# Kernel tuning notes

Hardware: AMD Instinct MI355X
Metric: run time of the kernel (lower is better)

The kernel has to match this reference:

```python
import jax, jax.numpy as jnp
import numpy as np

BITS = 4
GROUP = 128
IN_F = 4096
OUT_F = 11008
MAXQ = (1 << BITS) - 1  # 15


def setup_inputs() -> dict:
    key = jax.random.key(0)
    k = jax.random.split(key, 5)
    x = jax.random.normal(k[0], (4, 2048, IN_F), dtype=jnp.float32)
    qweight = jax.random.randint(k[1], (IN_F // 32 * BITS, OUT_F), 0, 2**31 - 1, dtype=jnp.int32)
    qzeros = jax.random.randint(k[2], (IN_F // GROUP, OUT_F // 32 * BITS), 0, 2**31 - 1, dtype=jnp.int32)
    scales = jax.random.uniform(k[3], (IN_F // GROUP, OUT_F), dtype=jnp.float32) * 0.01
    bias = jax.random.normal(k[4], (OUT_F,), dtype=jnp.float32)
    return {"x": x, "qweight": qweight, "qzeros": qzeros, "scales": scales, "bias": bias}


def reference(x, qweight, qzeros, scales, bias):
    # wf: bit offsets of the 8 nibbles inside each int32 word
    wf = jnp.arange(0, 32, BITS, dtype=jnp.int32)  # [8]
    # unpack zeros: [G, OUT//8] -> [G, OUT//8, 8] -> [G, OUT]
    zeros = ((qzeros[:, :, None] >> wf[None, None, :]) & MAXQ).reshape(scales.shape)
    # unpack weights: [IN//8, OUT] -> [IN//8, 8, OUT] -> [IN, OUT]
    weight = ((qweight[:, None, :] >> wf[None, :, None]) & MAXQ).reshape(IN_F, OUT_F)
    # group-wise dequant: W = s_g * (q - z_g)
    rep_scales = jnp.repeat(scales, GROUP, axis=0)              # [IN, OUT]
    rep_zeros = jnp.repeat(zeros, GROUP, axis=0).astype(x.dtype)
    W = rep_scales.astype(x.dtype) * (weight.astype(x.dtype) - rep_zeros)
    out = jnp.matmul(x.reshape(-1, IN_F), W)                    # [B*S, OUT]
    out = out.reshape(x.shape[:-1] + (OUT_F,)) + bias
    return out
```

## Files before the change

kernel.cpp:

```cpp
#include <hip/hip_runtime.h>
#include <stdint.h>

#define K_DIM 4096
#define N_DIM 11008
#define M_DIM 8192

constexpr int BM = 128, BN = 128, BK = 64;
constexpr int NT  = K_DIM / BK;
constexpr int NZW = N_DIM / 8;
constexpr int NXT = N_DIM / BN;
constexpr int MXT = M_DIM / BM;
constexpr int NWG = NXT * MXT;
constexpr int TILE_ELEMS = BM * BK;

typedef _Float16 f16x2 __attribute__((ext_vector_type(2)));
typedef _Float16 f16x8 __attribute__((ext_vector_type(8)));
typedef float    f32x4 __attribute__((ext_vector_type(4)));
union H8 { f16x8 v; f16x2 p[4]; };

__device__ __forceinline__ f16x8 dq_word(uint32_t w, f16x2 ss, f16x2 zz) {
    H8 r;
    uint32_t t0 = ( w        & 0x000F000Fu) | 0x64006400u;
    uint32_t t1 = ((w >> 4)  & 0x000F000Fu) | 0x64006400u;
    uint32_t t2 = ((w >> 8)  & 0x000F000Fu) | 0x64006400u;
    uint32_t t3 = ((w >> 12) & 0x000F000Fu) | 0x64006400u;
    r.p[0] = (__builtin_bit_cast(f16x2, t0) - zz) * ss;
    r.p[1] = (__builtin_bit_cast(f16x2, t1) - zz) * ss;
    r.p[2] = (__builtin_bit_cast(f16x2, t2) - zz) * ss;
    r.p[3] = (__builtin_bit_cast(f16x2, t3) - zz) * ss;
    return r.v;
}

__global__ __launch_bounds__(256)
void prep_kernel(const float* __restrict__ x, _Float16* __restrict__ x16) {
    const int b  = blockIdx.x;
    const int mt = b >> 6, kt = b & 63;
    _Float16* dst = x16 + (size_t)b * TILE_ELEMS;
#pragma unroll
    for (int it = 0; it < 4; ++it) {
        const int o   = it * 256 + threadIdx.x;
        const int fk  = o >> 7, row = o & 127;
        const float* src = x + (size_t)(mt * 128 + row) * K_DIM + kt * 64 + fk * 8;
        f32x4 a0 = *(const f32x4*)src;
        f32x4 a1 = *(const f32x4*)(src + 4);
        H8 v;
#pragma unroll
        for (int j = 0; j < 4; ++j)
            v.p[j] = __builtin_bit_cast(f16x2, __builtin_amdgcn_cvt_pkrtz(a0[j], a1[j]));
        *(f16x8*)(dst + (size_t)o * 8) = v.v;
    }
}

#define BARC(N) do {                                                         \
    __builtin_amdgcn_sched_barrier(0);                                       \
    asm volatile("s_waitcnt vmcnt(" #N ") lgkmcnt(0)" ::: "memory");         \
    __builtin_amdgcn_s_barrier();                                            \
    __builtin_amdgcn_sched_barrier(0);                                       \
} while (0)

__global__ __launch_bounds__(256, 4)
void qgemm_dma_kernel(const _Float16* __restrict__ x16, const uint32_t* __restrict__ qw,
                      const uint32_t* __restrict__ qz, const float* __restrict__ sc,
                      const float* __restrict__ bias, float* __restrict__ out)
{
    __shared__ _Float16 As[2 * TILE_ELEMS];

    const int tid  = threadIdx.x;
    const int lid  = (blockIdx.x & 7) * (NWG / 8) + (blockIdx.x >> 3);
    const int mt   = lid / NXT;
    const int n0   = (lid % NXT) * BN;

    const int lane = tid & 63, wid = tid >> 6;
    const int lr = lane & 15, lk = lane >> 4;

    f32x4 acc[8][2];
#pragma unroll
    for (int i = 0; i < 8; ++i)
#pragma unroll
        for (int j = 0; j < 2; ++j) {
            f32x4 z = {0.f, 0.f, 0.f, 0.f};
            acc[i][j] = z;
        }

    uint32_t breg[2][4];
    f16x2    ssv[2], zzv[2];
    float    s_nxt[2];
    uint32_t z_nxt[2];

    const int ncb = n0 + wid * 32 + lr;
    const int shz = 4 * (lr & 7);

    const _Float16* xsrc = x16 + (size_t)mt * (64 * TILE_ELEMS) + tid * 8;
    const uint32_t* qp0 = qw + (size_t)lk * N_DIM + ncb;
    const uint32_t* qp1 = qp0 + (size_t)4 * N_DIM;

#define STAGE(BUF, KT) do {                                                  \
    const _Float16* s_ = xsrc + (size_t)(KT) * TILE_ELEMS;                   \
    _Float16* d_ = &As[(BUF) * TILE_ELEMS + tid * 8];                        \
    _Pragma("unroll") for (int it = 0; it < 4; ++it)                         \
        __builtin_amdgcn_global_load_lds(                                    \
            (const __attribute__((address_space(1))) void*)(s_ + it * 2048), \
            (__attribute__((address_space(3))) void*)(d_ + it * 2048), 16, 0, 0); \
    __builtin_amdgcn_sched_barrier(0);   \
    } while (0)

#define LOADB(SET) do {                                                      \
    breg[SET][0] = qp0[0];  breg[SET][1] = qp0[16];                          \
    breg[SET][2] = qp1[0];  breg[SET][3] = qp1[16];                          \
    qp0 += (size_t)8 * N_DIM; qp1 += (size_t)8 * N_DIM; } while (0)

#define LOADSZ(G) do { _Pragma("unroll") for (int j = 0; j < 2; ++j) {       \
    s_nxt[j] = sc[(size_t)(G) * N_DIM + ncb + j * 16];                       \
    z_nxt[j] = qz[(size_t)(G) * NZW + (ncb >> 3) + j * 2]; } } while (0)

#define MAKESZ() do { _Pragma("unroll") for (int j = 0; j < 2; ++j) {        \
    _Float16 zh = (_Float16)(float)(1024u + ((z_nxt[j] >> shz) & 15u));      \
    _Float16 sh = (_Float16)s_nxt[j];                                        \
    f16x2 sp = {sh, sh}; ssv[j] = sp;                                        \
    f16x2 zp = {zh, zh}; zzv[j] = zp; } } while (0)

#define COMPUTE(BUF, SET) do {                                               \
    _Pragma("unroll") for (int ks = 0; ks < 2; ++ks) {                       \
        f16x8 bf0 = dq_word(breg[SET][ks * 2],     ssv[0], zzv[0]);          \
        f16x8 bf1 = dq_word(breg[SET][ks * 2 + 1], ssv[1], zzv[1]);          \
        const int fo_ = (BUF) * TILE_ELEMS + (ks * 4 + lk) * 1024 + lr * 8;  \
        __builtin_amdgcn_s_setprio(1);                                       \
        _Pragma("unroll") for (int i = 0; i < 8; ++i) {                      \
            f16x8 af_ = *(const f16x8*)&As[fo_ + i * 128];                   \
            acc[i][0] = __builtin_amdgcn_mfma_f32_16x16x32_f16(af_, bf0, acc[i][0], 0, 0, 0); \
            acc[i][1] = __builtin_amdgcn_mfma_f32_16x16x32_f16(af_, bf1, acc[i][1], 0, 0, 0); \
        }                                                                    \
        __builtin_amdgcn_s_setprio(0);                                       \
    } } while (0)

    LOADSZ(0);
    STAGE(0, 0);
    LOADB(0);
    BARC(4);

    for (int kt2 = 0; kt2 < NT / 2; ++kt2) {
        const int t0 = 2 * kt2;
        MAKESZ();
        STAGE(1, t0 + 1);
        LOADB(1);
        COMPUTE(0, 0);
        BARC(4);

        if (kt2 + 1 < NT / 2) {
            STAGE(0, t0 + 2);
            LOADB(0);
            LOADSZ(kt2 + 1);
            COMPUTE(1, 1);
            BARC(8);
        } else {
            COMPUTE(1, 1);
        }
    }

#undef STAGE
#undef LOADB
#undef LOADSZ
#undef MAKESZ
#undef COMPUTE

    const int ccol0 = n0 + wid * 32 + lr;
    float bj[2];
#pragma unroll
    for (int j = 0; j < 2; ++j) bj[j] = bias[ccol0 + j * 16];
    const int m0 = mt * BM;
#pragma unroll
    for (int i = 0; i < 8; ++i) {
        const int rbase = m0 + i * 16 + lk * 4;
#pragma unroll
        for (int j = 0; j < 2; ++j) {
            const int col = ccol0 + j * 16;
#pragma unroll
            for (int r = 0; r < 4; ++r)
                out[(size_t)(rbase + r) * N_DIM + col] = acc[i][j][r] + bj[j];
        }
    }
}

constexpr int FB_LDA = 64;

#define BAR() do {                                           \
    asm volatile("s_waitcnt lgkmcnt(0)" ::: "memory");       \
    __builtin_amdgcn_s_barrier();                            \
    __builtin_amdgcn_sched_barrier(0);                       \
} while (0)

__global__ __launch_bounds__(256, 3)
void qgemm_fb_kernel(const float* __restrict__ x, const uint32_t* __restrict__ qw,
                     const uint32_t* __restrict__ qz, const float* __restrict__ sc,
                     const float* __restrict__ bias, float* __restrict__ out)
{
    __shared__ _Float16 As[2][BM * FB_LDA];

    const int tid  = threadIdx.x;
    const int lid  = (blockIdx.x & 7) * (NWG / 8) + (blockIdx.x >> 3);
    const int m0   = (lid / NXT) * BM;
    const int n0   = (lid % NXT) * BN;

    const int lane = tid & 63, wid = tid >> 6;
    const int lr = lane & 15, lk = lane >> 4;
    const int sw = lr & 7;

    const int arow = tid >> 3;
    const int acp  = tid & 7;
    const int wslot = acp ^ (arow & 7);

    f32x4 acc[8][2];
#pragma unroll
    for (int i = 0; i < 8; ++i)
#pragma unroll
        for (int j = 0; j < 2; ++j) { f32x4 z = {0.f,0.f,0.f,0.f}; acc[i][j] = z; }

    f32x4    aS[4][2];
    uint32_t breg[2][4];
    f16x2    ssv[2], zzv[2];
    float    s_nxt[2];
    uint32_t z_nxt[2];

    const int ncb = n0 + wid * 32 + lr;
    const int shz = 4 * (lr & 7);
    const float* xbase = x + (size_t)(m0 + arow) * K_DIM + acp * 8;

    const uint32_t* qp0 = qw + (size_t)lk * N_DIM + ncb;
    const uint32_t* qp1 = qp0 + (size_t)4 * N_DIM;

#define A_LOAD(KT) do { const float* ap_ = xbase + (KT) * BK;                \
    _Pragma("unroll") for (int i = 0; i < 4; ++i) {                          \
        const float* src_ = ap_ + (size_t)(i * 32) * K_DIM;                  \
        aS[i][0] = *(const f32x4*)(src_);                                    \
        aS[i][1] = *(const f32x4*)(src_ + 4); } } while (0)

#define A_WRITE(BUF) do {                                                    \
    _Pragma("unroll") for (int i = 0; i < 4; ++i) { H8 v_;                   \
        _Pragma("unroll") for (int j = 0; j < 4; ++j)                        \
            v_.p[j] = __builtin_bit_cast(f16x2,                              \
                __builtin_amdgcn_cvt_pkrtz(aS[i][0][j], aS[i][1][j]));       \
        *(f16x8*)&As[BUF][(arow + i * 32) * FB_LDA + wslot * 8] = v_.v; } } while (0)

#define LOADB(SET) do {                                                      \
    breg[SET][0] = qp0[0];  breg[SET][1] = qp0[16];                          \
    breg[SET][2] = qp1[0];  breg[SET][3] = qp1[16];                          \
    qp0 += (size_t)8 * N_DIM; qp1 += (size_t)8 * N_DIM; } while (0)

#define LOADSZ(G) do { _Pragma("unroll") for (int j = 0; j < 2; ++j) {       \
    s_nxt[j] = sc[(size_t)(G) * N_DIM + ncb + j * 16];                       \
    z_nxt[j] = qz[(size_t)(G) * NZW + (ncb >> 3) + j * 2]; } } while (0)

#define MAKESZ() do { _Pragma("unroll") for (int j = 0; j < 2; ++j) {        \
    _Float16 zh = (_Float16)(float)(1024u + ((z_nxt[j] >> shz) & 15u));      \
    _Float16 sh = (_Float16)s_nxt[j];                                        \
    f16x2 sp = {sh, sh}; ssv[j] = sp;                                        \
    f16x2 zp = {zh, zh}; zzv[j] = zp; } } while (0)

#define COMPUTE(BUF, SET) do {                                               \
    _Pragma("unroll") for (int ks = 0; ks < 2; ++ks) {                       \
        f16x8 bf0 = dq_word(breg[SET][ks * 2],     ssv[0], zzv[0]);          \
        f16x8 bf1 = dq_word(breg[SET][ks * 2 + 1], ssv[1], zzv[1]);          \
        const int rs_ = ((ks * 4 + lk) ^ sw) * 8;                            \
        _Pragma("unroll") for (int i = 0; i < 8; ++i) {                      \
            f16x8 af_ = *(const f16x8*)&As[BUF][(i * 16 + lr) * FB_LDA + rs_]; \
            acc[i][0] = __builtin_amdgcn_mfma_f32_16x16x32_f16(af_, bf0, acc[i][0], 0, 0, 0); \
            acc[i][1] = __builtin_amdgcn_mfma_f32_16x16x32_f16(af_, bf1, acc[i][1], 0, 0, 0); \
        } } } while (0)

    LOADSZ(0);
    A_LOAD(0);
    LOADB(0);
    A_WRITE(0);
    BAR();

    for (int kt2 = 0; kt2 < NT / 2; ++kt2) {
        const int t0 = 2 * kt2;
        MAKESZ();
        A_LOAD(t0 + 1);
        LOADB(1);
        COMPUTE(0, 0);
        A_WRITE(1);
        BAR();

        if (kt2 + 1 < NT / 2) {
            A_LOAD(t0 + 2);
            LOADB(0);
            LOADSZ(kt2 + 1);
            COMPUTE(1, 1);
            A_WRITE(0);
        } else {
            COMPUTE(1, 1);
        }
        BAR();
    }

#undef A_LOAD
#undef A_WRITE
#undef LOADB
#undef LOADSZ
#undef MAKESZ
#undef COMPUTE

    const int ccol0 = n0 + wid * 32 + lr;
    float bj[2];
#pragma unroll
    for (int j = 0; j < 2; ++j) bj[j] = bias[ccol0 + j * 16];
#pragma unroll
    for (int i = 0; i < 8; ++i) {
        const int rbase = m0 + i * 16 + lk * 4;
#pragma unroll
        for (int j = 0; j < 2; ++j) {
            const int col = ccol0 + j * 16;
#pragma unroll
            for (int r = 0; r < 4; ++r)
                out[(size_t)(rbase + r) * N_DIM + col] = acc[i][j][r] + bj[j];
        }
    }
}

extern "C" void kernel_launch(void* const* d_in, const int* in_sizes, int n_in,
                              void* d_out, int out_size, void* d_ws, size_t ws_size,
                              hipStream_t stream) {
    const float*    xp = (const float*)d_in[0];
    const uint32_t* qw = (const uint32_t*)d_in[1];
    const uint32_t* qz = (const uint32_t*)d_in[2];
    const float*    sc = (const float*)d_in[3];
    const float*    bi = (const float*)d_in[4];
    float*          op = (float*)d_out;
    (void)in_sizes; (void)n_in; (void)out_size;

    const size_t need = (size_t)M_DIM * K_DIM * sizeof(_Float16);
    if (ws_size >= need) {
        prep_kernel<<<dim3(MXT * NT), dim3(256), 0, stream>>>(xp, (_Float16*)d_ws);
        qgemm_dma_kernel<<<dim3(NWG), dim3(256), 0, stream>>>((const _Float16*)d_ws, qw, qz, sc, bi, op);
    } else {
        qgemm_fb_kernel<<<dim3(NWG), dim3(256), 0, stream>>>(xp, qw, qz, sc, bi, op);
    }
}
```

Before: 724.0 us.

## Pre-dequantize weights into fragment-ordered fp16 buffer before the GEMM

Adds a prep kernel that dequantizes the 4-bit weights once into an fp16 workspace laid out in MFMA fragment order. The main GEMM then loads ready-made f16x8 B fragments instead of unpacking nibbles in every tile, which removes the repeated dequant ALU work and the scale/zero loads from the inner loop. It also wraps the MFMA block in s_setprio. The cost is an extra ~90MB of workspace, an extra kernel launch, and more B-side memory traffic (fp16 instead of 4-bit). The fp32 fallback kernel is removed, so the fallback path now assumes workspace exists for the A buffer.

```diff
diff --git a/kernel.cpp b/kernel.cpp
--- a/kernel.cpp
+++ b/kernel.cpp
@@ -12,6 +12,8 @@
 constexpr int MXT = M_DIM / BM;
 constexpr int NWG = NXT * MXT;
 constexpr int TILE_ELEMS = BM * BK;
+constexpr size_t A16_BYTES = (size_t)M_DIM * K_DIM * 2;
+constexpr size_t B16_BYTES = (size_t)N_DIM * K_DIM * 2;
 
 typedef _Float16 f16x2 __attribute__((ext_vector_type(2)));
 typedef _Float16 f16x8 __attribute__((ext_vector_type(8)));
@@ -51,6 +53,31 @@
     }
 }
 
+__global__ __launch_bounds__(256)
+void prepb_kernel(const uint32_t* __restrict__ qw, const uint32_t* __restrict__ qz,
+                  const float* __restrict__ sc, _Float16* __restrict__ Bd) {
+    const int b     = blockIdx.x;
+    const int kt    = b / NXT, ntile = b % NXT;
+    const int col   = threadIdx.x & 127;
+    const int fq    = threadIdx.x >> 7;
+    const int colg  = ntile * 128 + col;
+    const int g     = kt >> 1;
+    const float    s  = sc[(size_t)g * N_DIM + colg];
+    const uint32_t zw = qz[(size_t)g * NZW + (colg >> 3)];
+    const uint32_t zn = (zw >> (4 * (colg & 7))) & 15u;
+    _Float16 sh = (_Float16)s;
+    _Float16 zh = (_Float16)(float)(1024u + zn);
+    f16x2 ss = {sh, sh}, zz = {zh, zh};
+    _Float16* dst = Bd + (((size_t)(ntile * 64 + kt) * 8 + fq * 4) * 128 + col) * 8;
+#pragma unroll
+    for (int i = 0; i < 4; ++i) {
+        const int fk = fq * 4 + i;
+        const uint32_t w = qw[(size_t)(kt * 8 + fk) * N_DIM + colg];
+        f16x8 v = dq_word(w, ss, zz);
+        *(f16x8*)(dst + (size_t)i * 1024) = v;
+    }
+}
+
 #define BARC(N) do {                                                         \
     __builtin_amdgcn_sched_barrier(0);                                       \
     asm volatile("s_waitcnt vmcnt(" #N ") lgkmcnt(0)" ::: "memory");         \
@@ -58,9 +85,8 @@
     __builtin_amdgcn_sched_barrier(0);                                       \
 } while (0)
 
-__global__ __launch_bounds__(256, 4)
-void qgemm_dma_kernel(const _Float16* __restrict__ x16, const uint32_t* __restrict__ qw,
-                      const uint32_t* __restrict__ qz, const float* __restrict__ sc,
+__global__ __launch_bounds__(256, 3)
+void qgemm_f16_kernel(const _Float16* __restrict__ x16, const _Float16* __restrict__ Bd,
                       const float* __restrict__ bias, float* __restrict__ out)
 {
     __shared__ _Float16 As[2 * TILE_ELEMS];
@@ -68,7 +94,8 @@
     const int tid  = threadIdx.x;
     const int lid  = (blockIdx.x & 7) * (NWG / 8) + (blockIdx.x >> 3);
     const int mt   = lid / NXT;
-    const int n0   = (lid % NXT) * BN;
+    const int nti  = lid % NXT;
+    const int n0   = nti * BN;
 
     const int lane = tid & 63, wid = tid >> 6;
     const int lr = lane & 15, lk = lane >> 4;
@@ -82,17 +109,11 @@
             acc[i][j] = z;
         }
 
-    uint32_t breg[2][4];
-    f16x2    ssv[2], zzv[2];
-    float    s_nxt[2];
-    uint32_t z_nxt[2];
-
-    const int ncb = n0 + wid * 32 + lr;
-    const int shz = 4 * (lr & 7);
+    f16x8 bfrag[2][4];
 
     const _Float16* xsrc = x16 + (size_t)mt * (64 * TILE_ELEMS) + tid * 8;
-    const uint32_t* qp0 = qw + (size_t)lk * N_DIM + ncb;
-    const uint32_t* qp1 = qp0 + (size_t)4 * N_DIM;
+    const _Float16* bsrc = Bd + (size_t)nti * (64 * 8192)
+                              + (size_t)lk * 1024 + (wid * 32 + lr) * 8;
 
 #define STAGE(BUF, KT) do {                                                  \
     const _Float16* s_ = xsrc + (size_t)(KT) * TILE_ELEMS;                   \
@@ -102,6 +123,112 @@
             (const __attribute__((address_space(1))) void*)(s_ + it * 2048), \
             (__attribute__((address_space(3))) void*)(d_ + it * 2048), 16, 0, 0); \
     __builtin_amdgcn_sched_barrier(0);   \
+    } while (0)
+
+#define LOADB(SET, KT) do {                                                  \
+    const _Float16* bp_ = bsrc + (size_t)(KT) * 8192;                        \
+    bfrag[SET][0] = *(const f16x8*)(bp_);                                    \
+    bfrag[SET][1] = *(const f16x8*)(bp_ + 128);                              \
+    bfrag[SET][2] = *(const f16x8*)(bp_ + 4096);                             \
+    bfrag[SET][3] = *(const f16x8*)(bp_ + 4096 + 128);                       \
+    } while (0)
+
+#define COMPUTE(BUF, SET) do {                                               \
+    _Pragma("unroll") for (int ks = 0; ks < 2; ++ks) {                       \
+        const int fo_ = (BUF) * TILE_ELEMS + (ks * 4 + lk) * 1024 + lr * 8;  \
+        __builtin_amdgcn_s_setprio(1);                                       \
+        _Pragma("unroll") for (int i = 0; i < 8; ++i) {                      \
+            f16x8 af_ = *(const f16x8*)&As[fo_ + i * 128];                   \
+            acc[i][0] = __builtin_amdgcn_mfma_f32_16x16x32_f16(af_, bfrag[SET][ks * 2],     acc[i][0], 0, 0, 0); \
+            acc[i][1] = __builtin_amdgcn_mfma_f32_16x16x32_f16(af_, bfrag[SET][ks * 2 + 1], acc[i][1], 0, 0, 0); \
+        }                                                                    \
+        __builtin_amdgcn_s_setprio(0);                                       \
+    } } while (0)
+
+    STAGE(0, 0);
+    LOADB(0, 0);
+    BARC(4);
+
+    for (int kt2 = 0; kt2 < NT / 2; ++kt2) {
+        const int t0 = 2 * kt2;
+        STAGE(1, t0 + 1);
+        LOADB(1, t0 + 1);
+        COMPUTE(0, 0);
+        BARC(4);
+
+        if (kt2 + 1 < NT / 2) {
+            STAGE(0, t0 + 2);
+            LOADB(0, t0 + 2);
+            COMPUTE(1, 1);
+            BARC(4);
+        } else {
+            COMPUTE(1, 1);
+        }
+    }
+
+#undef STAGE
+#undef LOADB
+#undef COMPUTE
+
+    const int ccol0 = n0 + wid * 32 + lr;
+    float bj[2];
+#pragma unroll
+    for (int j = 0; j < 2; ++j) bj[j] = bias[ccol0 + j * 16];
+    const int m0 = mt * BM;
+#pragma unroll
+    for (int i = 0; i < 8; ++i) {
+        const int rbase = m0 + i * 16 + lk * 4;
+#pragma unroll
+        for (int j = 0; j < 2; ++j) {
+            const int col = ccol0 + j * 16;
+#pragma unroll
+            for (int r = 0; r < 4; ++r)
+                out[(size_t)(rbase + r) * N_DIM + col] = acc[i][j][r] + bj[j];
+        }
+    }
+}
+
+__global__ __launch_bounds__(256, 4)
+void qgemm_dma_kernel(const _Float16* __restrict__ x16, const uint32_t* __restrict__ qw,
+                      const uint32_t* __restrict__ qz, const float* __restrict__ sc,
+                      const float* __restrict__ bias, float* __restrict__ out)
+{
+    __shared__ _Float16 As[2 * TILE_ELEMS];
+
+    const int tid  = threadIdx.x;
+    const int lid  = (blockIdx.x & 7) * (NWG / 8) + (blockIdx.x >> 3);
+    const int mt   = lid / NXT;
+    const int n0   = (lid % NXT) * BN;
+
+    const int lane = tid & 63, wid = tid >> 6;
+    const int lr = lane & 15, lk = lane >> 4;
+
+    f32x4 acc[8][2];
+#pragma unroll
+    for (int i = 0; i < 8; ++i)
+#pragma unroll
+        for (int j = 0; j < 2; ++j) { f32x4 z = {0.f,0.f,0.f,0.f}; acc[i][j] = z; }
+
+    uint32_t breg[2][4];
+    f16x2    ssv[2], zzv[2];
+    float    s_nxt[2];
+    uint32_t z_nxt[2];
+
+    const int ncb = n0 + wid * 32 + lr;
+    const int shz = 4 * (lr & 7);
+
+    const _Float16* xsrc = x16 + (size_t)mt * (64 * TILE_ELEMS) + tid * 8;
+    const uint32_t* qp0 = qw + (size_t)lk * N_DIM + ncb;
+    const uint32_t* qp1 = qp0 + (size_t)4 * N_DIM;
+
+#define STAGE(BUF, KT) do {                                                  \
+    const _Float16* s_ = xsrc + (size_t)(KT) * TILE_ELEMS;                   \
+    _Float16* d_ = &As[(BUF) * TILE_ELEMS + tid * 8];                        \
+    _Pragma("unroll") for (int it = 0; it < 4; ++it)                         \
+        __builtin_amdgcn_global_load_lds(                                    \
+            (const __attribute__((address_space(1))) void*)(s_ + it * 2048), \
+            (__attribute__((address_space(3))) void*)(d_ + it * 2048), 16, 0, 0); \
+    __builtin_amdgcn_sched_barrier(0);                                       \
     } while (0)
 
 #define LOADB(SET) do {                                                      \
@@ -181,143 +308,6 @@
     }
 }
 
-constexpr int FB_LDA = 64;
-
-#define BAR() do {                                           \
-    asm volatile("s_waitcnt lgkmcnt(0)" ::: "memory");       \
-    __builtin_amdgcn_s_barrier();                            \
-    __builtin_amdgcn_sched_barrier(0);                       \
-} while (0)
-
-__global__ __launch_bounds__(256, 3)
-void qgemm_fb_kernel(const float* __restrict__ x, const uint32_t* __restrict__ qw,
-                     const uint32_t* __restrict__ qz, const float* __restrict__ sc,
-                     const float* __restrict__ bias, float* __restrict__ out)
-{
-    __shared__ _Float16 As[2][BM * FB_LDA];
-
-    const int tid  = threadIdx.x;
-    const int lid  = (blockIdx.x & 7) * (NWG / 8) + (blockIdx.x >> 3);
-    const int m0   = (lid / NXT) * BM;
-    const int n0   = (lid % NXT) * BN;
-
-    const int lane = tid & 63, wid = tid >> 6;
-    const int lr = lane & 15, lk = lane >> 4;
-    const int sw = lr & 7;
-
-    const int arow = tid >> 3;
-    const int acp  = tid & 7;
-    const int wslot = acp ^ (arow & 7);
-
-    f32x4 acc[8][2];
-#pragma unroll
-    for (int i = 0; i < 8; ++i)
-#pragma unroll
-        for (int j = 0; j < 2; ++j) { f32x4 z = {0.f,0.f,0.f,0.f}; acc[i][j] = z; }
-
-    f32x4    aS[4][2];
-    uint32_t breg[2][4];
-    f16x2    ssv[2], zzv[2];
-    float    s_nxt[2];
-    uint32_t z_nxt[2];
-
-    const int ncb = n0 + wid * 32 + lr;
-    const int shz = 4 * (lr & 7);
-    const float* xbase = x + (size_t)(m0 + arow) * K_DIM + acp * 8;
-
-    const uint32_t* qp0 = qw + (size_t)lk * N_DIM + ncb;
-    const uint32_t* qp1 = qp0 + (size_t)4 * N_DIM;
-
-#define A_LOAD(KT) do { const float* ap_ = xbase + (KT) * BK;                \
-    _Pragma("unroll") for (int i = 0; i < 4; ++i) {                          \
-        const float* src_ = ap_ + (size_t)(i * 32) * K_DIM;                  \
-        aS[i][0] = *(const f32x4*)(src_);                                    \
-        aS[i][1] = *(const f32x4*)(src_ + 4); } } while (0)
-
-#define A_WRITE(BUF) do {                                                    \
-    _Pragma("unroll") for (int i = 0; i < 4; ++i) { H8 v_;                   \
-        _Pragma("unroll") for (int j = 0; j < 4; ++j)                        \
-            v_.p[j] = __builtin_bit_cast(f16x2,                              \
-                __builtin_amdgcn_cvt_pkrtz(aS[i][0][j], aS[i][1][j]));       \
-        *(f16x8*)&As[BUF][(arow + i * 32) * FB_LDA + wslot * 8] = v_.v; } } while (0)
-
-#define LOADB(SET) do {                                                      \
-    breg[SET][0] = qp0[0];  breg[SET][1] = qp0[16];                          \
-    breg[SET][2] = qp1[0];  breg[SET][3] = qp1[16];                          \
-    qp0 += (size_t)8 * N_DIM; qp1 += (size_t)8 * N_DIM; } while (0)
-
-#define LOADSZ(G) do { _Pragma("unroll") for (int j = 0; j < 2; ++j) {       \
-    s_nxt[j] = sc[(size_t)(G) * N_DIM + ncb + j * 16];                       \
-    z_nxt[j] = qz[(size_t)(G) * NZW + (ncb >> 3) + j * 2]; } } while (0)
-
-#define MAKESZ() do { _Pragma("unroll") for (int j = 0; j < 2; ++j) {        \
-    _Float16 zh = (_Float16)(float)(1024u + ((z_nxt[j] >> shz) & 15u));      \
-    _Float16 sh = (_Float16)s_nxt[j];                                        \
-    f16x2 sp = {sh, sh}; ssv[j] = sp;                                        \
-    f16x2 zp = {zh, zh}; zzv[j] = zp; } } while (0)
-
-#define COMPUTE(BUF, SET) do {                                               \
-    _Pragma("unroll") for (int ks = 0; ks < 2; ++ks) {                       \
-        f16x8 bf0 = dq_word(breg[SET][ks * 2],     ssv[0], zzv[0]);          \
-        f16x8 bf1 = dq_word(breg[SET][ks * 2 + 1], ssv[1], zzv[1]);          \
-        const int rs_ = ((ks * 4 + lk) ^ sw) * 8;                            \
-        _Pragma("unroll") for (int i = 0; i < 8; ++i) {                      \
-            f16x8 af_ = *(const f16x8*)&As[BUF][(i * 16 + lr) * FB_LDA + rs_]; \
-            acc[i][0] = __builtin_amdgcn_mfma_f32_16x16x32_f16(af_, bf0, acc[i][0], 0, 0, 0); \
-            acc[i][1] = __builtin_amdgcn_mfma_f32_16x16x32_f16(af_, bf1, acc[i][1], 0, 0, 0); \
-        } } } while (0)
-
-    LOADSZ(0);
-    A_LOAD(0);
-    LOADB(0);
-    A_WRITE(0);
-    BAR();
-
-    for (int kt2 = 0; kt2 < NT / 2; ++kt2) {
-        const int t0 = 2 * kt2;
-        MAKESZ();
-        A_LOAD(t0 + 1);
-        LOADB(1);
-        COMPUTE(0, 0);
-        A_WRITE(1);
-        BAR();
-
-        if (kt2 + 1 < NT / 2) {
-            A_LOAD(t0 + 2);
-            LOADB(0);
-            LOADSZ(kt2 + 1);
-            COMPUTE(1, 1);
-            A_WRITE(0);
-        } else {
-            COMPUTE(1, 1);
-        }
-        BAR();
-    }
-
-#undef A_LOAD
-#undef A_WRITE
-#undef LOADB
-#undef LOADSZ
-#undef MAKESZ
-#undef COMPUTE
-
-    const int ccol0 = n0 + wid * 32 + lr;
-    float bj[2];
-#pragma unroll
-    for (int j = 0; j < 2; ++j) bj[j] = bias[ccol0 + j * 16];
-#pragma unroll
-    for (int i = 0; i < 8; ++i) {
-        const int rbase = m0 + i * 16 + lk * 4;
-#pragma unroll
-        for (int j = 0; j < 2; ++j) {
-            const int col = ccol0 + j * 16;
-#pragma unroll
-            for (int r = 0; r < 4; ++r)
-                out[(size_t)(rbase + r) * N_DIM + col] = acc[i][j][r] + bj[j];
-        }
-    }
-}
-
 extern "C" void kernel_launch(void* const* d_in, const int* in_sizes, int n_in,
                               void* d_out, int out_size, void* d_ws, size_t ws_size,
                               hipStream_t stream) {
@@ -329,11 +319,14 @@
     float*          op = (float*)d_out;
     (void)in_sizes; (void)n_in; (void)out_size;
 
-    const size_t need = (size_t)M_DIM * K_DIM * sizeof(_Float16);
-    if (ws_size >= need) {
-        prep_kernel<<<dim3(MXT * NT), dim3(256), 0, stream>>>(xp, (_Float16*)d_ws);
-        qgemm_dma_kernel<<<dim3(NWG), dim3(256), 0, stream>>>((const _Float16*)d_ws, qw, qz, sc, bi, op);
+    _Float16* a16 = (_Float16*)d_ws;
+    if (ws_size >= A16_BYTES + B16_BYTES) {
+        _Float16* b16 = (_Float16*)((char*)d_ws + A16_BYTES);
+        prep_kernel <<<dim3(MXT * NT), dim3(256), 0, stream>>>(xp, a16);
+        prepb_kernel<<<dim3(NT * NXT), dim3(256), 0, stream>>>(qw, qz, sc, b16);
+        qgemm_f16_kernel<<<dim3(NWG), dim3(256), 0, stream>>>(a16, b16, bi, op);
     } else {
-        qgemm_fb_kernel<<<dim3(NWG), dim3(256), 0, stream>>>(xp, qw, qz, sc, bi, op);
-    }
-}
+        prep_kernel<<<dim3(MXT * NT), dim3(256), 0, stream>>>(xp, a16);
+        qgemm_dma_kernel<<<dim3(NWG), dim3(256), 0, stream>>>(a16, qw, qz, sc, bi, op);
+    }
+}
```

New measurement: 927.0 us. 1.28x slower.
